# Performance work log

Measured on AMD Instinct MI355X. Metric: run time of the kernel, lower is better.

Reference implementation:

```python
import jax, jax.numpy as jnp
import numpy as np

R = 4  # box radius (init kwarg r)


def setup_inputs() -> dict:
    key = jax.random.key(0)
    x = jax.random.normal(key, (8, 16, 512, 512), dtype=jnp.float32)
    return {"x": x}


def reference(x) -> jnp.ndarray:
    r = R
    # Integral image: pad (r+1 before, r after) on H and W, then double cumsum.
    summed = jnp.pad(x, ((0, 0), (0, 0), (r + 1, r), (r + 1, r)))
    summed = jnp.cumsum(jnp.cumsum(summed, axis=2), axis=3)
    k = 2 * r + 1
    intersection = summed[:, :, :-k, :-k]
    union = summed[:, :, k:, k:]
    left = summed[:, :, :-k, k:]
    right = summed[:, :, k:, :-k]
    return union - left - right + intersection
```

## Files before the change

### kernel.cpp

```cpp
#include <hip/hip_runtime.h>


#define W   512
#define RR  16
#define NSTRIP (W / RR)

__device__ __forceinline__ float4 ld4(const float* p) { return *(const float4*)p; }
__device__ __forceinline__ float4 add4(float4 a, float4 b) {
    return make_float4(a.x + b.x, a.y + b.y, a.z + b.z, a.w + b.w);
}
__device__ __forceinline__ float4 sub4(float4 a, float4 b) {
    return make_float4(a.x - b.x, a.y - b.y, a.z - b.z, a.w - b.w);
}

__global__ __launch_bounds__(256, 4) void boxfilter9(const float* __restrict__ in,
                                                     float* __restrict__ out) {
    const int t     = threadIdx.x;
    const int unit  = blockIdx.x * 2 + (t >> 7);
    const int img   = unit / NSTRIP;
    const int strip = unit % NSTRIP;
    const int cg    = t & 127;
    const int c0    = cg << 2;

    const float* __restrict__ inp  = in  + (size_t)img * W * W;
    float* __restrict__       outp = out + (size_t)img * W * W;
    const int  y0    = strip * RR;
    const bool has_l = (c0 >= 4);
    const bool has_r = (c0 + 4 < W);

    auto compute_h = [&](int y) -> float4 {
        float4 h;
        if ((unsigned)y < W) {
            const float* row = inp + y * W;
            float4 a = has_l ? ld4(row + c0 - 4) : make_float4(0, 0, 0, 0);
            float4 b = ld4(row + c0);
            float4 c = has_r ? ld4(row + c0 + 4) : make_float4(0, 0, 0, 0);
            float s0 = ((a.x + a.y) + (a.z + a.w)) +
                       (((b.x + b.y) + (b.z + b.w)) + c.x);
            h.x = s0;
            h.y = s0  - a.x + c.y;
            h.z = h.y - a.y + c.z;
            h.w = h.z - a.z + c.w;
        } else {
            h = make_float4(0, 0, 0, 0);
        }
        return h;
    };

    float4 ring[9];
    float4 vsum = make_float4(0, 0, 0, 0);
    #pragma unroll
    for (int k = 0; k < 8; ++k) {
        ring[k] = compute_h(y0 - 4 + k);
        vsum = add4(vsum, ring[k]);
    }

    #pragma unroll
    for (int i = 0; i < RR; ++i) {
        float4 hn = compute_h(y0 + 4 + i);
        float4 o  = add4(vsum, hn);
        *(float4*)(outp + (size_t)(y0 + i) * W + c0) = o;
        vsum = sub4(o, ring[i % 9]);
        ring[(i + 8) % 9] = hn;
    }
}

extern "C" void kernel_launch(void* const* d_in, const int* in_sizes, int n_in,
                              void* d_out, int out_size, void* d_ws, size_t ws_size,
                              hipStream_t stream) {
    const float* x = (const float*)d_in[0];
    float* y = (float*)d_out;
    dim3 grid(128 * NSTRIP / 2);
    dim3 block(256);
    boxfilter9<<<grid, block, 0, stream>>>(x, y);
}
```

Baseline: 256.1 us.

## Use DPP lane shifts so each wave covers a full row of 8 floats per lane

Each wavefront now handles one full 512-wide row strip, with each lane owning 8 contiguous columns. The left and right neighbour columns come from adjacent lanes through DPP row shifts instead of extra overlapping global loads. This removes the redundant neighbour loads, which tripled read traffic per row, at the cost of DPP instructions and twice the ring-buffer registers. The DPP row_shr/shl ops work within 16-lane rows with bound_ctrl zero-fill, so columns at the 16-lane boundaries (every 128 floats) would get zeros instead of neighbour data. That looks wrong except at the image edges, and row_shr:1 probably also has the wrong direction.

```diff
diff --git a/kernel.cpp b/kernel.cpp
--- a/kernel.cpp
+++ b/kernel.cpp
@@ -13,55 +13,80 @@
     return make_float4(a.x - b.x, a.y - b.y, a.z - b.z, a.w - b.w);
 }
 
+__device__ __forceinline__ float lane_shr1(float x) {
+    return __int_as_float(__builtin_amdgcn_update_dpp(
+        0, __float_as_int(x), 0x138 , 0xF, 0xF, true));
+}
+__device__ __forceinline__ float lane_shl1(float x) {
+    return __int_as_float(__builtin_amdgcn_update_dpp(
+        0, __float_as_int(x), 0x130 , 0xF, 0xF, true));
+}
+__device__ __forceinline__ float4 lane_shr1_4(float4 v) {
+    return make_float4(lane_shr1(v.x), lane_shr1(v.y), lane_shr1(v.z), lane_shr1(v.w));
+}
+__device__ __forceinline__ float4 lane_shl1_4(float4 v) {
+    return make_float4(lane_shl1(v.x), lane_shl1(v.y), lane_shl1(v.z), lane_shl1(v.w));
+}
+
 __global__ __launch_bounds__(256, 4) void boxfilter9(const float* __restrict__ in,
                                                      float* __restrict__ out) {
     const int t     = threadIdx.x;
-    const int unit  = blockIdx.x * 2 + (t >> 7);
-    const int img   = unit / NSTRIP;
-    const int strip = unit % NSTRIP;
-    const int cg    = t & 127;
-    const int c0    = cg << 2;
+    const int l     = t & 63;
+    const int wid   = t >> 6;
+    const int unit  = blockIdx.x * 4 + wid;
+    const int img   = unit >> 5;
+    const int strip = unit & (NSTRIP - 1);
 
     const float* __restrict__ inp  = in  + (size_t)img * W * W;
     float* __restrict__       outp = out + (size_t)img * W * W;
-    const int  y0    = strip * RR;
-    const bool has_l = (c0 >= 4);
-    const bool has_r = (c0 + 4 < W);
+    const int y0 = strip * RR;
+    const int c0 = l << 3;
 
-    auto compute_h = [&](int y) -> float4 {
-        float4 h;
+    auto compute_h = [&](int y, float4& h0, float4& h1) {
         if ((unsigned)y < W) {
-            const float* row = inp + y * W;
-            float4 a = has_l ? ld4(row + c0 - 4) : make_float4(0, 0, 0, 0);
-            float4 b = ld4(row + c0);
-            float4 c = has_r ? ld4(row + c0 + 4) : make_float4(0, 0, 0, 0);
-            float s0 = ((a.x + a.y) + (a.z + a.w)) +
-                       (((b.x + b.y) + (b.z + b.w)) + c.x);
-            h.x = s0;
-            h.y = s0  - a.x + c.y;
-            h.z = h.y - a.y + c.z;
-            h.w = h.z - a.z + c.w;
+            const float* row = inp + y * W + c0;
+            float4 lo = ld4(row);
+            float4 hi = ld4(row + 4);
+            float4 ap = lane_shr1_4(hi);
+            float4 an = lane_shl1_4(lo);
+            float sa = (ap.x + ap.y) + (ap.z + ap.w);
+            float sl = (lo.x + lo.y) + (lo.z + lo.w);
+            h0.x = (sa + sl) + hi.x;
+            h0.y = h0.x - ap.x + hi.y;
+            h0.z = h0.y - ap.y + hi.z;
+            h0.w = h0.z - ap.z + hi.w;
+            h1.x = h0.w - ap.w + an.x;
+            h1.y = h1.x - lo.x + an.y;
+            h1.z = h1.y - lo.y + an.z;
+            h1.w = h1.z - lo.z + an.w;
         } else {
-            h = make_float4(0, 0, 0, 0);
+            h0 = make_float4(0, 0, 0, 0);
+            h1 = make_float4(0, 0, 0, 0);
         }
-        return h;
     };
 
-    float4 ring[9];
-    float4 vsum = make_float4(0, 0, 0, 0);
+    float4 ring0[9], ring1[9];
+    float4 vs0 = make_float4(0, 0, 0, 0), vs1 = make_float4(0, 0, 0, 0);
     #pragma unroll
     for (int k = 0; k < 8; ++k) {
-        ring[k] = compute_h(y0 - 4 + k);
-        vsum = add4(vsum, ring[k]);
+        compute_h(y0 - 4 + k, ring0[k], ring1[k]);
+        vs0 = add4(vs0, ring0[k]);
+        vs1 = add4(vs1, ring1[k]);
     }
 
     #pragma unroll
     for (int i = 0; i < RR; ++i) {
-        float4 hn = compute_h(y0 + 4 + i);
-        float4 o  = add4(vsum, hn);
-        *(float4*)(outp + (size_t)(y0 + i) * W + c0) = o;
-        vsum = sub4(o, ring[i % 9]);
-        ring[(i + 8) % 9] = hn;
+        float4 hn0, hn1;
+        compute_h(y0 + 4 + i, hn0, hn1);
+        float4 o0 = add4(vs0, hn0);
+        float4 o1 = add4(vs1, hn1);
+        float* orow = outp + (size_t)(y0 + i) * W + c0;
+        *(float4*)(orow)     = o0;
+        *(float4*)(orow + 4) = o1;
+        vs0 = sub4(o0, ring0[i % 9]);
+        vs1 = sub4(o1, ring1[i % 9]);
+        ring0[(i + 8) % 9] = hn0;
+        ring1[(i + 8) % 9] = hn1;
     }
 }
 
@@ -70,7 +95,7 @@
                               hipStream_t stream) {
     const float* x = (const float*)d_in[0];
     float* y = (float*)d_out;
-    dim3 grid(128 * NSTRIP / 2);
+    dim3 grid(128 * NSTRIP / 4);
     dim3 block(256);
     boxfilter9<<<grid, block, 0, stream>>>(x, y);
 }
```

New measurement: 309.5 us. 20.9% more time.
